# Performance work log

Hardware: AMD Instinct MI355X
Metric: run time of the kernel (lower is better)

## Reference

```python
import jax, jax.numpy as jnp
import numpy as np

M, K, N = 8192, 4096, 4096


def setup_inputs() -> dict:
    key = jax.random.key(0)
    k1, k2, k3, k4, k5 = jax.random.split(key, 5)
    x = jax.random.randint(k1, (M, K), -127, 128, dtype=jnp.int32).astype(jnp.int8)
    weight_int8 = jax.random.randint(k2, (N, K), -127, 128, dtype=jnp.int32).astype(jnp.int8)
    scale_x = jax.random.uniform(k3, (M,), dtype=jnp.float32, minval=0.001, maxval=0.02)
    scale_w = jnp.abs(jax.random.normal(k4, (N,), dtype=jnp.float32)) * 0.01
    bias = (jax.random.normal(k5, (N,), dtype=jnp.float32) * 0.01).astype(jnp.float16)
    return {"x": x, "scale_x": scale_x, "weight_int8": weight_int8,
            "scale_w": scale_w, "bias": bias}


def reference(x, scale_x, weight_int8, scale_w, bias):
    # int8 GEMM with int32 accumulation: acc[M,N] = x @ weight^T
    acc = jnp.matmul(x, weight_int8.T, preferred_element_type=jnp.int32)
    inv_127_sq = jnp.float32(1.0 / (127.0 * 127.0))
    scale_w_eff = scale_w * inv_127_sq                      # [N]
    out = acc.astype(jnp.float32) * scale_x[:, None] * scale_w_eff[None, :]
    out = out + bias.astype(jnp.float32)[None, :]
    return out.astype(jnp.float16)
```

## Files before the change

kernel.cpp:

```cpp
#include <hip/hip_runtime.h>
#include <stdint.h>

#define M_DIM 8192
#define K_DIM 4096
#define N_DIM 4096

typedef __attribute__((ext_vector_type(4))) int v4i;

__device__ __forceinline__ int pack4(v4i v) {
    return (int)(((uint32_t)v.x & 0xffu)
               | (((uint32_t)v.y & 0xffu) << 8)
               | (((uint32_t)v.z & 0xffu) << 16)
               | (((uint32_t)v.w & 0xffu) << 24));
}

__global__ __launch_bounds__(256) void pack_ab(
    const int* __restrict__ srcA, const int* __restrict__ srcB,
    int* __restrict__ dstA, int* __restrict__ dstB,
    int aGroups)
{
    int g = blockIdx.x * 256 + threadIdx.x;
    const v4i* src;
    int* dst;
    if (g < aGroups) { src = (const v4i*)srcA; dst = dstA; }
    else             { src = (const v4i*)srcB; dst = dstB; g -= aGroups; }
    dst[g] = pack4(src[g]);
}

__device__ __forceinline__ void gload16(const void* g, void* lds_p) {
    __builtin_amdgcn_global_load_lds(
        (__attribute__((address_space(1))) void*)(g),
        (__attribute__((address_space(3))) void*)(lds_p),
        16, 0, 0);
}

__global__ __launch_bounds__(512, 2) void int8_gemm_dequant(
    const int8_t* __restrict__ A,
    const float*  __restrict__ scale_x,
    const int8_t* __restrict__ W,
    const float*  __restrict__ scale_w,
    const float*  __restrict__ bias,
    float*        __restrict__ out)
{
    __shared__ __align__(16) int8_t lds[131072];

    const int t    = threadIdx.x;
    const int lane = t & 63;
    const int w    = t >> 6;
    const int wm   = w >> 2;
    const int wn   = w & 3;

    const int wg  = blockIdx.x;
    const int swz = (wg & 7) * 64 + (wg >> 3);
    const int n0  = (swz & 15) * 256;
    const int m0  = (swz >> 4) * 256;

    const int srow = t >> 2;
    const int scg  = (t & 3) ^ ((t >> 3) & 3);
    const int8_t* Ap = A + (size_t)(m0 + srow) * K_DIM + scg * 16;
    const int8_t* Bp = W + (size_t)(n0 + srow) * K_DIM + scg * 16;
    int8_t* ldsb = &lds[t * 16];

    const int rd = (lane & 15) * 64 + (((lane >> 4) ^ ((lane >> 1) & 3)) * 16);

    v4i acc[8][4] = {};
    v4i afr[4], bfr[4];

#define HOFF(buf, mat, ksh) ((((buf) << 2) | ((mat) << 1) | (ksh)) << 14)

#define STAGE(buf, mat, ksh, OFF) do {                                        \
    const int8_t* _g = ((mat) ? Bp : Ap) + (OFF) + (ksh) * 64;                \
    int8_t* _d = ldsb + HOFF(buf, mat, ksh);                                  \
    gload16(_g, _d);                                                          \
    gload16(_g + (size_t)128 * K_DIM, _d + 8192);                             \
} while (0)

#define READ_B(buf, ksh) do {                                                 \
    const int8_t* _p = lds + HOFF(buf, 1, ksh) + wn * 4096 + rd;              \
    bfr[0] = *(const v4i*)(_p);                                               \
    bfr[1] = *(const v4i*)(_p + 1024);                                        \
    bfr[2] = *(const v4i*)(_p + 2048);                                        \
    bfr[3] = *(const v4i*)(_p + 3072);                                        \
} while (0)

#define READ_A(buf, ksh, qm) do {                                             \
    const int8_t* _p = lds + HOFF(buf, 0, ksh) + wm * 8192 + (qm) * 4096 + rd;\
    afr[0] = *(const v4i*)(_p);                                               \
    afr[1] = *(const v4i*)(_p + 1024);                                        \
    afr[2] = *(const v4i*)(_p + 2048);                                        \
    afr[3] = *(const v4i*)(_p + 3072);                                        \
} while (0)

#define MFMA_Q(qm) do {                                                       \
    _Pragma("unroll")                                                         \
    for (int mt = 0; mt < 4; ++mt) {                                          \
        _Pragma("unroll")                                                     \
        for (int nt = 0; nt < 4; ++nt) {                                      \
            acc[(qm) * 4 + mt][nt] = __builtin_amdgcn_mfma_i32_16x16x64_i8(   \
                afr[mt], bfr[nt], acc[(qm) * 4 + mt][nt], 0, 0, 0);           \
        }                                                                     \
    }                                                                         \
} while (0)

#define NOWAIT ((void)0)
#define WAIT4  asm volatile("s_waitcnt vmcnt(4)" ::: "memory")
#define WAIT0  asm volatile("s_waitcnt vmcnt(0)" ::: "memory")
#define NOSTG  ((void)0)

#define PHASE(DO_RB, buf, ksh, qm, STG, WAITV) do {                           \
    if (DO_RB) { READ_B(buf, ksh); }                                          \
    READ_A(buf, ksh, qm);                                                     \
    STG;                                                                      \
    WAITV;                                                                    \
    __builtin_amdgcn_s_barrier();                                             \
    asm volatile("s_waitcnt lgkmcnt(0)" ::: "memory");                        \
    __builtin_amdgcn_s_setprio(1);                                            \
    MFMA_Q(qm);                                                               \
    __builtin_amdgcn_s_setprio(0);                                            \
} while (0)

    STAGE(0, 1, 0, 0);   STAGE(0, 0, 0, 0);
    STAGE(0, 1, 1, 0);   STAGE(0, 0, 1, 0);
    STAGE(1, 1, 0, 128); STAGE(1, 0, 0, 128);
    WAIT4;
    __builtin_amdgcn_s_barrier();

    for (int i = 0; i < 15; ++i) {
        PHASE(1, 0, 0, 0, STAGE(1, 1, 1, 128), NOWAIT);
        PHASE(0, 0, 0, 1, STAGE(1, 0, 1, 128), NOWAIT);
        PHASE(1, 0, 1, 0, STAGE(0, 1, 0, 256), NOWAIT);
        PHASE(0, 0, 1, 1, STAGE(0, 0, 0, 256), WAIT4);
        PHASE(1, 1, 0, 0, STAGE(0, 1, 1, 256), NOWAIT);
        PHASE(0, 1, 0, 1, STAGE(0, 0, 1, 256), NOWAIT);
        PHASE(1, 1, 1, 0, STAGE(1, 1, 0, 384), NOWAIT);
        PHASE(0, 1, 1, 1, STAGE(1, 0, 0, 384), WAIT4);
        Ap += 256; Bp += 256;
    }

    PHASE(1, 0, 0, 0, STAGE(1, 1, 1, 128), NOWAIT);
    PHASE(0, 0, 0, 1, STAGE(1, 0, 1, 128), NOWAIT);
    PHASE(1, 0, 1, 0, NOSTG, NOWAIT);
    PHASE(0, 0, 1, 1, NOSTG, WAIT0);
    PHASE(1, 1, 0, 0, NOSTG, NOWAIT);
    PHASE(0, 1, 0, 1, NOSTG, NOWAIT);
    PHASE(1, 1, 1, 0, NOSTG, NOWAIT);
    PHASE(0, 1, 1, 1, NOSTG, NOWAIT);

    const int col = lane & 15;
    const int rq  = (lane >> 4) * 4;
    const float inv127sq = 1.0f / (127.0f * 127.0f);
    const int mbase = m0 + wm * 128;
    const int nbase = n0 + wn * 64;

    float sx[8][4];
#pragma unroll
    for (int ii = 0; ii < 8; ++ii) {
        const int mrow = mbase + (ii >> 2) * 64 + (ii & 3) * 16 + rq;
#pragma unroll
        for (int r = 0; r < 4; ++r) sx[ii][r] = scale_x[mrow + r];
    }

#pragma unroll
    for (int j = 0; j < 4; ++j) {
        const int n  = nbase + j * 16 + col;
        const float sw = scale_w[n] * inv127sq;
        const float bf = bias[n];
#pragma unroll
        for (int ii = 0; ii < 8; ++ii) {
            const int mrow = mbase + (ii >> 2) * 64 + (ii & 3) * 16 + rq;
#pragma unroll
            for (int r = 0; r < 4; ++r) {
                out[(size_t)(mrow + r) * N_DIM + n] =
                    (float)acc[ii][j][r] * sx[ii][r] * sw + bf;
            }
        }
    }

#undef HOFF
#undef STAGE
#undef READ_B
#undef READ_A
#undef MFMA_Q
#undef NOWAIT
#undef WAIT4
#undef WAIT0
#undef NOSTG
#undef PHASE
}

extern "C" void kernel_launch(void* const* d_in, const int* in_sizes, int n_in,
                              void* d_out, int out_size, void* d_ws, size_t ws_size,
                              hipStream_t stream) {
    const int*   x_i32   = (const int*)  d_in[0];
    const float* scale_x = (const float*)d_in[1];
    const int*   w_i32   = (const int*)  d_in[2];
    const float* scale_w = (const float*)d_in[3];
    const float* bias    = (const float*)d_in[4];
    float* out = (float*)d_out;

    int8_t* A8 = (int8_t*)d_ws;
    int8_t* B8 = A8 + (size_t)M_DIM * K_DIM;

    const int a_groups = (M_DIM * K_DIM) / 4;
    const int b_groups = (N_DIM * K_DIM) / 4;
    const int total    = a_groups + b_groups;
    pack_ab<<<total / 256, 256, 0, stream>>>(x_i32, w_i32, (int*)A8, (int*)B8,
                                             a_groups);

    int8_gemm_dequant<<<512, 512, 0, stream>>>(A8, scale_x, B8, scale_w, bias, out);
}
```

Before: 399.0 us.

## Double-buffer MFMA operand registers to prefetch LDS fragments during compute

Splits the A and B operand fragments into two register sets. Each phase now issues the next phase's LDS reads right after the barrier and then runs the current phase's MFMAs, instead of reading and waiting on lgkmcnt(0) before computing. The aim is to hide LDS read latency behind matrix-core work. In exchange it adds 32 live VGPRs under a 512-thread, 2-blocks-per-CU launch bound, which risks spills or lower occupancy, and it relies on compiler-inserted waits in place of the explicit one.

```diff
diff --git a/kernel.cpp b/kernel.cpp
--- a/kernel.cpp
+++ b/kernel.cpp
@@ -64,7 +64,7 @@
     const int rd = (lane & 15) * 64 + (((lane >> 4) ^ ((lane >> 1) & 3)) * 16);
 
     v4i acc[8][4] = {};
-    v4i afr[4], bfr[4];
+    v4i afr0[4], afr1[4], bfr0[4], bfr1[4];
 
 #define HOFF(buf, mat, ksh) ((((buf) << 2) | ((mat) << 1) | (ksh)) << 14)
 
@@ -75,29 +75,29 @@
     gload16(_g + (size_t)128 * K_DIM, _d + 8192);                             \
 } while (0)
 
-#define READ_B(buf, ksh) do {                                                 \
+#define READ_B_TO(DST, buf, ksh) do {                                         \
     const int8_t* _p = lds + HOFF(buf, 1, ksh) + wn * 4096 + rd;              \
-    bfr[0] = *(const v4i*)(_p);                                               \
-    bfr[1] = *(const v4i*)(_p + 1024);                                        \
-    bfr[2] = *(const v4i*)(_p + 2048);                                        \
-    bfr[3] = *(const v4i*)(_p + 3072);                                        \
-} while (0)
-
-#define READ_A(buf, ksh, qm) do {                                             \
+    DST[0] = *(const v4i*)(_p);                                               \
+    DST[1] = *(const v4i*)(_p + 1024);                                        \
+    DST[2] = *(const v4i*)(_p + 2048);                                        \
+    DST[3] = *(const v4i*)(_p + 3072);                                        \
+} while (0)
+
+#define READ_A_TO(DST, buf, ksh, qm) do {                                     \
     const int8_t* _p = lds + HOFF(buf, 0, ksh) + wm * 8192 + (qm) * 4096 + rd;\
-    afr[0] = *(const v4i*)(_p);                                               \
-    afr[1] = *(const v4i*)(_p + 1024);                                        \
-    afr[2] = *(const v4i*)(_p + 2048);                                        \
-    afr[3] = *(const v4i*)(_p + 3072);                                        \
-} while (0)
-
-#define MFMA_Q(qm) do {                                                       \
+    DST[0] = *(const v4i*)(_p);                                               \
+    DST[1] = *(const v4i*)(_p + 1024);                                        \
+    DST[2] = *(const v4i*)(_p + 2048);                                        \
+    DST[3] = *(const v4i*)(_p + 3072);                                        \
+} while (0)
+
+#define MFMA_Q(qm, AF, BF) do {                                               \
     _Pragma("unroll")                                                         \
     for (int mt = 0; mt < 4; ++mt) {                                          \
         _Pragma("unroll")                                                     \
         for (int nt = 0; nt < 4; ++nt) {                                      \
             acc[(qm) * 4 + mt][nt] = __builtin_amdgcn_mfma_i32_16x16x64_i8(   \
-                afr[mt], bfr[nt], acc[(qm) * 4 + mt][nt], 0, 0, 0);           \
+                AF[mt], BF[nt], acc[(qm) * 4 + mt][nt], 0, 0, 0);             \
         }                                                                     \
     }                                                                         \
 } while (0)
@@ -106,16 +106,16 @@
 #define WAIT4  asm volatile("s_waitcnt vmcnt(4)" ::: "memory")
 #define WAIT0  asm volatile("s_waitcnt vmcnt(0)" ::: "memory")
 #define NOSTG  ((void)0)
-
-#define PHASE(DO_RB, buf, ksh, qm, STG, WAITV) do {                           \
-    if (DO_RB) { READ_B(buf, ksh); }                                          \
-    READ_A(buf, ksh, qm);                                                     \
+#define NORD   ((void)0)
+
+#define PH(qm, AF, BF, NEXTRD, STG, WAITV) do {                               \
     STG;                                                                      \
     WAITV;                                                                    \
     __builtin_amdgcn_s_barrier();                                             \
-    asm volatile("s_waitcnt lgkmcnt(0)" ::: "memory");                        \
+    NEXTRD;                                                                   \
+    __builtin_amdgcn_sched_barrier(0);                                        \
     __builtin_amdgcn_s_setprio(1);                                            \
-    MFMA_Q(qm);                                                               \
+    MFMA_Q(qm, AF, BF);                                                       \
     __builtin_amdgcn_s_setprio(0);                                            \
 } while (0)
 
@@ -124,27 +124,47 @@
     STAGE(1, 1, 0, 128); STAGE(1, 0, 0, 128);
     WAIT4;
     __builtin_amdgcn_s_barrier();
+    READ_A_TO(afr0, 0, 0, 0);
+    READ_B_TO(bfr0, 0, 0);
 
     for (int i = 0; i < 15; ++i) {
-        PHASE(1, 0, 0, 0, STAGE(1, 1, 1, 128), NOWAIT);
-        PHASE(0, 0, 0, 1, STAGE(1, 0, 1, 128), NOWAIT);
-        PHASE(1, 0, 1, 0, STAGE(0, 1, 0, 256), NOWAIT);
-        PHASE(0, 0, 1, 1, STAGE(0, 0, 0, 256), WAIT4);
-        PHASE(1, 1, 0, 0, STAGE(0, 1, 1, 256), NOWAIT);
-        PHASE(0, 1, 0, 1, STAGE(0, 0, 1, 256), NOWAIT);
-        PHASE(1, 1, 1, 0, STAGE(1, 1, 0, 384), NOWAIT);
-        PHASE(0, 1, 1, 1, STAGE(1, 0, 0, 384), WAIT4);
+        PH(0, afr0, bfr0, READ_A_TO(afr1, 0, 0, 1),
+           STAGE(1, 1, 1, 128), NOWAIT);
+        PH(1, afr1, bfr0,
+           { READ_A_TO(afr0, 0, 1, 0); READ_B_TO(bfr1, 0, 1); },
+           STAGE(1, 0, 1, 128), NOWAIT);
+        PH(0, afr0, bfr1, READ_A_TO(afr1, 0, 1, 1),
+           STAGE(0, 1, 0, 256), NOWAIT);
+        PH(1, afr1, bfr1,
+           { READ_A_TO(afr0, 1, 0, 0); READ_B_TO(bfr0, 1, 0); },
+           STAGE(0, 0, 0, 256), WAIT4);
+        PH(0, afr0, bfr0, READ_A_TO(afr1, 1, 0, 1),
+           STAGE(0, 1, 1, 256), NOWAIT);
+        PH(1, afr1, bfr0,
+           { READ_A_TO(afr0, 1, 1, 0); READ_B_TO(bfr1, 1, 1); },
+           STAGE(0, 0, 1, 256), NOWAIT);
+        PH(0, afr0, bfr1, READ_A_TO(afr1, 1, 1, 1),
+           STAGE(1, 1, 0, 384), NOWAIT);
+        PH(1, afr1, bfr1,
+           { READ_A_TO(afr0, 0, 0, 0); READ_B_TO(bfr0, 0, 0); },
+           STAGE(1, 0, 0, 384), WAIT4);
         Ap += 256; Bp += 256;
     }
 
-    PHASE(1, 0, 0, 0, STAGE(1, 1, 1, 128), NOWAIT);
-    PHASE(0, 0, 0, 1, STAGE(1, 0, 1, 128), NOWAIT);
-    PHASE(1, 0, 1, 0, NOSTG, NOWAIT);
-    PHASE(0, 0, 1, 1, NOSTG, WAIT0);
-    PHASE(1, 1, 0, 0, NOSTG, NOWAIT);
-    PHASE(0, 1, 0, 1, NOSTG, NOWAIT);
-    PHASE(1, 1, 1, 0, NOSTG, NOWAIT);
-    PHASE(0, 1, 1, 1, NOSTG, NOWAIT);
+    PH(0, afr0, bfr0, READ_A_TO(afr1, 0, 0, 1), STAGE(1, 1, 1, 128), NOWAIT);
+    PH(1, afr1, bfr0,
+       { READ_A_TO(afr0, 0, 1, 0); READ_B_TO(bfr1, 0, 1); },
+       STAGE(1, 0, 1, 128), NOWAIT);
+    PH(0, afr0, bfr1, READ_A_TO(afr1, 0, 1, 1), NOSTG, NOWAIT);
+    PH(1, afr1, bfr1,
+       { READ_A_TO(afr0, 1, 0, 0); READ_B_TO(bfr0, 1, 0); },
+       NOSTG, WAIT0);
+    PH(0, afr0, bfr0, READ_A_TO(afr1, 1, 0, 1), NOSTG, NOWAIT);
+    PH(1, afr1, bfr0,
+       { READ_A_TO(afr0, 1, 1, 0); READ_B_TO(bfr1, 1, 1); },
+       NOSTG, NOWAIT);
+    PH(0, afr0, bfr1, READ_A_TO(afr1, 1, 1, 1), NOSTG, NOWAIT);
+    PH(1, afr1, bfr1, NORD, NOSTG, NOWAIT);
 
     const int col = lane & 15;
     const int rq  = (lane >> 4) * 4;
@@ -178,14 +198,15 @@
 
 #undef HOFF
 #undef STAGE
-#undef READ_B
-#undef READ_A
+#undef READ_B_TO
+#undef READ_A_TO
 #undef MFMA_Q
 #undef NOWAIT
 #undef WAIT4
 #undef WAIT0
 #undef NOSTG
-#undef PHASE
+#undef NORD
+#undef PH
 }
 
 extern "C" void kernel_launch(void* const* d_in, const int* in_sizes, int n_in,
```

After: 395.5 us. Within noise of the previous version (-0.9%).

## Switch to 32x32x32 int8 MFMA with double-buffered register fragments

Applied to the files above, without the earlier changes.

Replaces the 16x16x64 int8 MFMA tiling with 32x32x32 MFMA tiles, so each wave reads fewer LDS fragments per unit of work. Fragment registers are now double-buffered so the LDS reads for the next k-chunk are issued right after the barrier, before the current MFMAs run. This drops the explicit lgkmcnt(0) wait and relies on the compiler to insert the dependency waits. The epilogue is rewritten for the 32x32 accumulator layout. Risks are higher register pressure from the extra fragment buffer and a read-after-barrier ordering that needs to stay correct.

```diff
diff --git a/kernel.cpp b/kernel.cpp
--- a/kernel.cpp
+++ b/kernel.cpp
@@ -5,7 +5,8 @@
 #define K_DIM 4096
 #define N_DIM 4096
 
-typedef __attribute__((ext_vector_type(4))) int v4i;
+typedef __attribute__((ext_vector_type(4)))  int v4i;
+typedef __attribute__((ext_vector_type(16))) int v16i;
 
 __device__ __forceinline__ int pack4(v4i v) {
     return (int)(((uint32_t)v.x & 0xffu)
@@ -61,10 +62,10 @@
     const int8_t* Bp = W + (size_t)(n0 + srow) * K_DIM + scg * 16;
     int8_t* ldsb = &lds[t * 16];
 
-    const int rd = (lane & 15) * 64 + (((lane >> 4) ^ ((lane >> 1) & 3)) * 16);
-
-    v4i acc[8][4] = {};
-    v4i afr[4], bfr[4];
+    const int rdb = (lane & 31) * 64 + ((((lane >> 5) ^ ((lane >> 1) & 3))) * 16);
+
+    v16i acc[4][2] = {};
+    v4i a0[4], a1[4], b0[2], b1[2];
 
 #define HOFF(buf, mat, ksh) ((((buf) << 2) | ((mat) << 1) | (ksh)) << 14)
 
@@ -75,29 +76,26 @@
     gload16(_g + (size_t)128 * K_DIM, _d + 8192);                             \
 } while (0)
 
-#define READ_B(buf, ksh) do {                                                 \
-    const int8_t* _p = lds + HOFF(buf, 1, ksh) + wn * 4096 + rd;              \
-    bfr[0] = *(const v4i*)(_p);                                               \
-    bfr[1] = *(const v4i*)(_p + 1024);                                        \
-    bfr[2] = *(const v4i*)(_p + 2048);                                        \
-    bfr[3] = *(const v4i*)(_p + 3072);                                        \
-} while (0)
-
-#define READ_A(buf, ksh, qm) do {                                             \
-    const int8_t* _p = lds + HOFF(buf, 0, ksh) + wm * 8192 + (qm) * 4096 + rd;\
-    afr[0] = *(const v4i*)(_p);                                               \
-    afr[1] = *(const v4i*)(_p + 1024);                                        \
-    afr[2] = *(const v4i*)(_p + 2048);                                        \
-    afr[3] = *(const v4i*)(_p + 3072);                                        \
-} while (0)
-
-#define MFMA_Q(qm) do {                                                       \
+#define READ_F(AS, BS, buf, ksh, kc) do {                                     \
+    const int8_t* _pa = lds + HOFF(buf, 0, ksh) + wm * 8192                   \
+                        + (rdb ^ ((kc) * 32));                                \
+    AS[0] = *(const v4i*)(_pa);                                               \
+    AS[1] = *(const v4i*)(_pa + 2048);                                        \
+    AS[2] = *(const v4i*)(_pa + 4096);                                        \
+    AS[3] = *(const v4i*)(_pa + 6144);                                        \
+    const int8_t* _pb = lds + HOFF(buf, 1, ksh) + wn * 4096                   \
+                        + (rdb ^ ((kc) * 32));                                \
+    BS[0] = *(const v4i*)(_pb);                                               \
+    BS[1] = *(const v4i*)(_pb + 2048);                                        \
+} while (0)
+
+#define MFMA_C(AF, BF) do {                                                   \
     _Pragma("unroll")                                                         \
     for (int mt = 0; mt < 4; ++mt) {                                          \
         _Pragma("unroll")                                                     \
-        for (int nt = 0; nt < 4; ++nt) {                                      \
-            acc[(qm) * 4 + mt][nt] = __builtin_amdgcn_mfma_i32_16x16x64_i8(   \
-                afr[mt], bfr[nt], acc[(qm) * 4 + mt][nt], 0, 0, 0);           \
+        for (int nt = 0; nt < 2; ++nt) {                                      \
+            acc[mt][nt] = __builtin_amdgcn_mfma_i32_32x32x32_i8(              \
+                AF[mt], BF[nt], acc[mt][nt], 0, 0, 0);                        \
         }                                                                     \
     }                                                                         \
 } while (0)
@@ -106,16 +104,16 @@
 #define WAIT4  asm volatile("s_waitcnt vmcnt(4)" ::: "memory")
 #define WAIT0  asm volatile("s_waitcnt vmcnt(0)" ::: "memory")
 #define NOSTG  ((void)0)
-
-#define PHASE(DO_RB, buf, ksh, qm, STG, WAITV) do {                           \
-    if (DO_RB) { READ_B(buf, ksh); }                                          \
-    READ_A(buf, ksh, qm);                                                     \
+#define NORD   ((void)0)
+
+#define PH(AF, BF, NEXTRD, STG, WAITV) do {                                   \
     STG;                                                                      \
     WAITV;                                                                    \
     __builtin_amdgcn_s_barrier();                                             \
-    asm volatile("s_waitcnt lgkmcnt(0)" ::: "memory");                        \
+    NEXTRD;                                                                   \
+    __builtin_amdgcn_sched_barrier(0);                                        \
     __builtin_amdgcn_s_setprio(1);                                            \
-    MFMA_Q(qm);                                                               \
+    MFMA_C(AF, BF);                                                           \
     __builtin_amdgcn_s_setprio(0);                                            \
 } while (0)
 
@@ -124,68 +122,64 @@
     STAGE(1, 1, 0, 128); STAGE(1, 0, 0, 128);
     WAIT4;
     __builtin_amdgcn_s_barrier();
+    READ_F(a0, b0, 0, 0, 0);
 
     for (int i = 0; i < 15; ++i) {
-        PHASE(1, 0, 0, 0, STAGE(1, 1, 1, 128), NOWAIT);
-        PHASE(0, 0, 0, 1, STAGE(1, 0, 1, 128), NOWAIT);
-        PHASE(1, 0, 1, 0, STAGE(0, 1, 0, 256), NOWAIT);
-        PHASE(0, 0, 1, 1, STAGE(0, 0, 0, 256), WAIT4);
-        PHASE(1, 1, 0, 0, STAGE(0, 1, 1, 256), NOWAIT);
-        PHASE(0, 1, 0, 1, STAGE(0, 0, 1, 256), NOWAIT);
-        PHASE(1, 1, 1, 0, STAGE(1, 1, 0, 384), NOWAIT);
-        PHASE(0, 1, 1, 1, STAGE(1, 0, 0, 384), WAIT4);
+        PH(a0, b0, READ_F(a1, b1, 0, 0, 1), STAGE(1, 1, 1, 128), NOWAIT);
+        PH(a1, b1, READ_F(a0, b0, 0, 1, 0), STAGE(1, 0, 1, 128), NOWAIT);
+        PH(a0, b0, READ_F(a1, b1, 0, 1, 1), STAGE(0, 1, 0, 256), NOWAIT);
+        PH(a1, b1, READ_F(a0, b0, 1, 0, 0), STAGE(0, 0, 0, 256), WAIT4);
+        PH(a0, b0, READ_F(a1, b1, 1, 0, 1), STAGE(0, 1, 1, 256), NOWAIT);
+        PH(a1, b1, READ_F(a0, b0, 1, 1, 0), STAGE(0, 0, 1, 256), NOWAIT);
+        PH(a0, b0, READ_F(a1, b1, 1, 1, 1), STAGE(1, 1, 0, 384), NOWAIT);
+        PH(a1, b1, READ_F(a0, b0, 0, 0, 0), STAGE(1, 0, 0, 384), WAIT4);
         Ap += 256; Bp += 256;
     }
 
-    PHASE(1, 0, 0, 0, STAGE(1, 1, 1, 128), NOWAIT);
-    PHASE(0, 0, 0, 1, STAGE(1, 0, 1, 128), NOWAIT);
-    PHASE(1, 0, 1, 0, NOSTG, NOWAIT);
-    PHASE(0, 0, 1, 1, NOSTG, WAIT0);
-    PHASE(1, 1, 0, 0, NOSTG, NOWAIT);
-    PHASE(0, 1, 0, 1, NOSTG, NOWAIT);
-    PHASE(1, 1, 1, 0, NOSTG, NOWAIT);
-    PHASE(0, 1, 1, 1, NOSTG, NOWAIT);
-
-    const int col = lane & 15;
-    const int rq  = (lane >> 4) * 4;
+    PH(a0, b0, READ_F(a1, b1, 0, 0, 1), STAGE(1, 1, 1, 128), NOWAIT);
+    PH(a1, b1, READ_F(a0, b0, 0, 1, 0), STAGE(1, 0, 1, 128), NOWAIT);
+    PH(a0, b0, READ_F(a1, b1, 0, 1, 1), NOSTG, NOWAIT);
+    PH(a1, b1, READ_F(a0, b0, 1, 0, 0), NOSTG, WAIT0);
+    PH(a0, b0, READ_F(a1, b1, 1, 0, 1), NOSTG, NOWAIT);
+    PH(a1, b1, READ_F(a0, b0, 1, 1, 0), NOSTG, NOWAIT);
+    PH(a0, b0, READ_F(a1, b1, 1, 1, 1), NOSTG, NOWAIT);
+    PH(a1, b1, NORD, NOSTG, NOWAIT);
+
+    const int colL = lane & 31;
+    const int rhi  = (lane >> 5) * 4;
     const float inv127sq = 1.0f / (127.0f * 127.0f);
     const int mbase = m0 + wm * 128;
     const int nbase = n0 + wn * 64;
 
-    float sx[8][4];
+    const int   nA = nbase + colL;
+    const int   nB = nbase + 32 + colL;
+    const float swA = scale_w[nA] * inv127sq;
+    const float swB = scale_w[nB] * inv127sq;
+    const float bfA = bias[nA];
+    const float bfB = bias[nB];
+
 #pragma unroll
-    for (int ii = 0; ii < 8; ++ii) {
-        const int mrow = mbase + (ii >> 2) * 64 + (ii & 3) * 16 + rq;
+    for (int mt = 0; mt < 4; ++mt) {
 #pragma unroll
-        for (int r = 0; r < 4; ++r) sx[ii][r] = scale_x[mrow + r];
-    }
-
-#pragma unroll
-    for (int j = 0; j < 4; ++j) {
-        const int n  = nbase + j * 16 + col;
-        const float sw = scale_w[n] * inv127sq;
-        const float bf = bias[n];
-#pragma unroll
-        for (int ii = 0; ii < 8; ++ii) {
-            const int mrow = mbase + (ii >> 2) * 64 + (ii & 3) * 16 + rq;
-#pragma unroll
-            for (int r = 0; r < 4; ++r) {
-                out[(size_t)(mrow + r) * N_DIM + n] =
-                    (float)acc[ii][j][r] * sx[ii][r] * sw + bf;
-            }
+        for (int reg = 0; reg < 16; ++reg) {
+            const int row = mbase + mt * 32 + (reg & 3) + 8 * (reg >> 2) + rhi;
+            const float s = scale_x[row];
+            float* orow = out + (size_t)row * N_DIM;
+            orow[nA] = (float)acc[mt][0][reg] * s * swA + bfA;
+            orow[nB] = (float)acc[mt][1][reg] * s * swB + bfB;
         }
     }
 
 #undef HOFF
 #undef STAGE
-#undef READ_B
-#undef READ_A
-#undef MFMA_Q
+#undef READ_F
+#undef MFMA_C
 #undef NOWAIT
 #undef WAIT4
 #undef WAIT0
 #undef NOSTG
-#undef PHASE
+#undef NORD
+#undef PH
 }
 
 extern "C" void kernel_launch(void* const* d_in, const int* in_sizes, int n_in,
```

New measurement: 400.0 us. Within noise of the previous version (+0.2%).
